# Optimization experiments

Measured on AMD Instinct MI355X. Metric: run time of the kernel, lower is better.

The kernel has to match this reference:

```python
import jax, jax.numpy as jnp
import numpy as np
import math

B, S, DIM = 2, 2048, 2048
H, KV, HD = 16, 1, 128  # query heads, kv heads, head dim


def setup_inputs() -> dict:
    key = jax.random.key(0)
    ks = jax.random.split(key, 6)
    std = 0.02
    return {
        "hidden_states": jax.random.normal(ks[0], (B, S, DIM), jnp.float32),
        "attention_mask": jnp.zeros((B, 1, S, S), jnp.float32),
        "wq": jax.random.normal(ks[1], (DIM, H * HD), jnp.float32) * std,
        "bq": jnp.zeros((H * HD,), jnp.float32),
        "wk": jax.random.normal(ks[2], (DIM, KV * HD), jnp.float32) * std,
        "bk": jnp.zeros((KV * HD,), jnp.float32),
        "wv": jax.random.normal(ks[3], (DIM, KV * HD), jnp.float32) * std,
        "bv": jnp.zeros((KV * HD,), jnp.float32),
        "wo": jax.random.normal(ks[4], (H * HD, DIM), jnp.float32) * std,
        "bo": jnp.zeros((DIM,), jnp.float32),
    }


def reference(hidden_states, attention_mask, wq, bq, wk, bk, wv, bv, wo, bo):
    b, s, _ = hidden_states.shape
    q = (hidden_states @ wq + bq).reshape(b, s, H, HD)
    k = (hidden_states @ wk + bk).reshape(b, s, KV, HD)
    v = (hidden_states @ wv + bv).reshape(b, s, KV, HD)
    # [b, h, s, d]
    q = jnp.transpose(q, (0, 2, 1, 3))
    k = jnp.transpose(k, (0, 2, 1, 3))
    v = jnp.transpose(v, (0, 2, 1, 3))
    # broadcast shared KV heads to all query heads (num_kv_heads < num_query_heads)
    repeats = H // KV
    k = jnp.repeat(k, repeats, axis=1)
    v = jnp.repeat(v, repeats, axis=1)
    scores = jnp.einsum('bhqd,bhkd->bhqk', q, k) / math.sqrt(HD)
    scores = scores + attention_mask
    weights = jax.nn.softmax(scores, axis=-1)
    attn = jnp.einsum('bhqk,bhkd->bhqd', weights, v)
    attn = jnp.transpose(attn, (0, 2, 1, 3)).reshape(b, s, H * HD)
    return attn @ wo + bo
```

## Files before the change

### kernel.cpp

```cpp
#include <hip/hip_runtime.h>
#include <hip/hip_bf16.h>
#include <stdint.h>

#define S_LEN 2048
#define DIMSZ 2048
#define NH    16
#define HD    128
#define NQK   2176
#define NQKV  2304

typedef short  bf16x8  __attribute__((ext_vector_type(8)));
typedef float  floatx4 __attribute__((ext_vector_type(4)));
typedef float  floatx16 __attribute__((ext_vector_type(16)));
typedef int    intx4   __attribute__((ext_vector_type(4)));
typedef unsigned short u16;

#define mfma32 __builtin_amdgcn_mfma_f32_32x32x16_bf16

__device__ __forceinline__ u16 f2bf(float x) {
  unsigned int u = __builtin_bit_cast(unsigned int, x);
  u = (u + 0x7FFFu + ((u >> 16) & 1u)) >> 16;
  return (u16)u;
}

__device__ __forceinline__ int cvtpk(float lo, float hi) {
  int r;
  asm("v_cvt_pk_bf16_f32 %0, %1, %2" : "=v"(r) : "v"(lo), "v"(hi));
  return r;
}

__device__ __forceinline__ void half_swap(int& a, int& b, int lane) {
  int as = __shfl_xor(a, 32);
  int bs = __shfl_xor(b, 32);
  int na = (lane < 32) ? a : bs;
  int nb = (lane < 32) ? as : b;
  a = na; b = nb;
}

__device__ __forceinline__ void gload16(const void* g, void* l) {
  __builtin_amdgcn_global_load_lds(
      reinterpret_cast<const __attribute__((address_space(1))) void*>(reinterpret_cast<uintptr_t>(g)),
      reinterpret_cast<__attribute__((address_space(3))) void*>(reinterpret_cast<uintptr_t>(l)),
      16, 0, 0);
}

__global__ void k_cvt_bf16(const float* __restrict__ in, u16* __restrict__ out, int n4) {
  int i = blockIdx.x * blockDim.x + threadIdx.x;
  if (i < n4) {
    float4 v = ((const float4*)in)[i];
    ushort4 o;
    o.x = f2bf(v.x); o.y = f2bf(v.y); o.z = f2bf(v.z); o.w = f2bf(v.w);
    ((ushort4*)out)[i] = o;
  }
}

__global__ void k_transpose_bf16(const float* __restrict__ in, u16* __restrict__ out,
                                 int K, int N, int rowOff) {
  __shared__ float t[64][65];
  int c0 = blockIdx.x * 64;
  int r0 = blockIdx.y * 64;
  int tid = threadIdx.x;
  int lr = tid >> 6;
  int lc = tid & 63;
#pragma unroll
  for (int i = 0; i < 16; ++i) {
    int r = lr + i * 4;
    t[r][lc] = in[(size_t)(r0 + r) * N + c0 + lc];
  }
  __syncthreads();
#pragma unroll
  for (int i = 0; i < 16; ++i) {
    int r = lr + i * 4;
    out[(size_t)(rowOff + c0 + r) * K + r0 + lc] = f2bf(t[lc][r]);
  }
}

__global__ void k_bias_concat(const float* __restrict__ bq, const float* __restrict__ bk,
                              const float* __restrict__ bv, float* __restrict__ out) {
  int i = blockIdx.x * 256 + threadIdx.x;
  if (i < NQKV) out[i] = (i < 2048) ? bq[i] : (i < NQK ? bk[i - 2048] : bv[i - NQK]);
}

__device__ __forceinline__ void stage_tile(const u16* __restrict__ G, int ldg, int row0, int kt,
                                           u16* lbase, int wid, int lane) {
#pragma unroll
  for (int i = 0; i < 4; ++i) {
    int c   = (wid * 4 + i) * 64 + lane;
    int row = c >> 3, cin = c & 7;
    int cs  = cin ^ (row & 7);
    const u16* g = G + (size_t)(row0 + row) * ldg + kt * 64 + cs * 8;
    gload16(g, (char*)lbase + (wid * 4 + i) * 1024);
  }
}

template <int OMODE>
__global__ __launch_bounds__(256)
void k_gemm(const u16* __restrict__ A, const u16* __restrict__ Bt,
            const float* __restrict__ bias, void* __restrict__ Cout,
            u16* __restrict__ vt, int M, int N, int K) {
  __shared__ u16 lA[2][128 * 64];
  __shared__ u16 lB[2][128 * 64];
  const int tid = threadIdx.x, lane = tid & 63, wid = tid >> 6;
  const int wm = wid >> 1, wn = wid & 1;
  const int tm = blockIdx.x, tn = blockIdx.y;
  const int nk = K >> 6;

  stage_tile(A, K, tm * 128, 0, lA[0], wid, lane);
  stage_tile(Bt, K, tn * 128, 0, lB[0], wid, lane);
  __syncthreads();

  floatx4 acc[4][4] = {};
  int buf = 0;
  for (int kt = 0; kt < nk; ++kt) {
    if (kt + 1 < nk) {
      stage_tile(A, K, tm * 128, kt + 1, lA[buf ^ 1], wid, lane);
      stage_tile(Bt, K, tn * 128, kt + 1, lB[buf ^ 1], wid, lane);
    }
    const char* pa = (const char*)&lA[buf][0];
    const char* pb = (const char*)&lB[buf][0];
#pragma unroll
    for (int kk = 0; kk < 2; ++kk) {
      bf16x8 af[4], bfr[4];
      int gch = kk * 4 + (lane >> 4);
#pragma unroll
      for (int f = 0; f < 4; ++f) {
        int ra = wm * 64 + f * 16 + (lane & 15);
        af[f]  = *(const bf16x8*)(pa + ra * 128 + ((gch ^ (ra & 7)) << 4));
        int rb = wn * 64 + f * 16 + (lane & 15);
        bfr[f] = *(const bf16x8*)(pb + rb * 128 + ((gch ^ (rb & 7)) << 4));
      }
#pragma unroll
      for (int fm = 0; fm < 4; ++fm)
#pragma unroll
        for (int fn = 0; fn < 4; ++fn)
          acc[fm][fn] = __builtin_amdgcn_mfma_f32_16x16x32_bf16(af[fm], bfr[fn], acc[fm][fn], 0, 0, 0);
    }
    __syncthreads();
    buf ^= 1;
  }

#pragma unroll
  for (int fm = 0; fm < 4; ++fm)
#pragma unroll
    for (int fn = 0; fn < 4; ++fn)
#pragma unroll
      for (int r = 0; r < 4; ++r) {
        int rowg = tm * 128 + wm * 64 + fm * 16 + (lane >> 4) * 4 + r;
        int colg = tn * 128 + wn * 64 + fn * 16 + (lane & 15);
        float v = acc[fm][fn][r] + bias[colg];
        if constexpr (OMODE == 1) {
          ((float*)Cout)[(size_t)rowg * N + colg] = v;
        } else {
          if (colg < NQK) {
            ((u16*)Cout)[(size_t)rowg * N + colg] = f2bf(v);
          } else {
            int d = colg - NQK;
            int bg = rowg >> 11, s = rowg & 2047;
            vt[((size_t)bg * HD + d) * S_LEN + s] = f2bf(v);
          }
        }
      }
}

__device__ __forceinline__ void stage_kv(const u16* __restrict__ qkv, const u16* __restrict__ vt,
                                         int b, int kt, u16* lK, u16* lV, int wid, int lane) {
#pragma unroll
  for (int i = 0; i < 2; ++i) {
    int seg = wid * 2 + i;
    {
      int r = seg * 4 + (lane >> 4), cin = lane & 15;
      const u16* g = qkv + (size_t)(b * S_LEN + kt * 64 + r) * NQKV + 2048 + ((cin ^ (r & 7)) * 8);
      gload16(g, (char*)lK + seg * 1024);
    }
    {
      int r = seg * 8 + (lane >> 3), cin = lane & 7;
      const u16* g = vt + ((size_t)b * HD + r) * S_LEN + kt * 64 + ((cin ^ (r & 7)) * 8);
      gload16(g, (char*)lV + seg * 1024);
    }
  }
}

__global__ __launch_bounds__(512)
void k_attn(const u16* __restrict__ qkv, const u16* __restrict__ vt,
            const float* __restrict__ mask, u16* __restrict__ attn) {
  __shared__ __align__(16) u16   lK[2][64 * 128];
  __shared__ __align__(16) u16   lV[2][128 * 64];
  __shared__ __align__(16) float lM[2][32 * 64];
  const int tid = threadIdx.x, lane = tid & 63, wid = tid >> 6;
  const int qt = blockIdx.x, hg = blockIdx.y, b = blockIdx.z;
  const int h = hg * 8 + wid;
  const int q = lane & 31, h5 = lane >> 5;
  const float scale = 0.08838834764831845f;

  bf16x8 qf[8];
  const size_t qrow = (size_t)(b * S_LEN + qt * 32 + q);
#pragma unroll
  for (int cs = 0; cs < 8; ++cs)
    qf[cs] = *(const bf16x8*)(qkv + qrow * NQKV + h * HD + cs * 16 + h5 * 8);

  float m_ = -1e30f, l_ = 0.f;
  floatx16 acco[4] = {};

  const int mq = tid >> 4, mc = tid & 15;
  const float* mrow = mask + (size_t)b * S_LEN * S_LEN + (size_t)(qt * 32 + mq) * S_LEN + mc * 4;

  stage_kv(qkv, vt, b, 0, lK[0], lV[0], wid, lane);
  floatx4 mreg = *(const floatx4*)(mrow);
  *(floatx4*)((char*)&lM[0][0] + mq * 256 + ((mc ^ (mq & 7)) << 4)) = mreg;
  __syncthreads();

  int buf = 0;
  for (int kt = 0; kt < S_LEN / 64; ++kt) {
    if (kt + 1 < S_LEN / 64) {
      stage_kv(qkv, vt, b, kt + 1, lK[buf ^ 1], lV[buf ^ 1], wid, lane);
      mreg = *(const floatx4*)(mrow + (size_t)(kt + 1) * 64);
    }

    floatx16 accs0 = {}, accs1 = {};
    const char* pK = (const char*)&lK[buf][0];
#pragma unroll
    for (int cs = 0; cs < 8; ++cs) {
      int c = cs * 2 + h5;
      bf16x8 kf0 = *(const bf16x8*)(pK + q * 256 + ((c ^ (q & 7)) << 4));
      bf16x8 kf1 = *(const bf16x8*)(pK + (32 + q) * 256 + 8192 - 8192 + ((c ^ (q & 7)) << 4));
      accs0 = mfma32(kf0, qf[cs], accs0, 0, 0, 0);
      accs1 = mfma32(kf1, qf[cs], accs1, 0, 0, 0);
    }

    float pr[32];
    float rowm = -1e30f;
    const char* pM = (const char*)&lM[buf][0];
#pragma unroll
    for (int kb = 0; kb < 2; ++kb)
#pragma unroll
      for (int rg = 0; rg < 4; ++rg) {
        int c = kb * 8 + rg * 2 + h5;
        floatx4 m4 = *(const floatx4*)(pM + q * 256 + ((c ^ (q & 7)) << 4));
#pragma unroll
        for (int t = 0; t < 4; ++t) {
          float sv = (kb ? accs1[rg * 4 + t] : accs0[rg * 4 + t]) * scale + m4[t];
          pr[kb * 16 + rg * 4 + t] = sv;
          rowm = fmaxf(rowm, sv);
        }
      }
    rowm = fmaxf(rowm, __shfl_xor(rowm, 32));
    float mn = fmaxf(m_, rowm);
    float al = __expf(m_ - mn);
    m_ = mn;
    float sum = 0.f;
#pragma unroll
    for (int j = 0; j < 32; ++j) {
      float e = __expf(pr[j] - mn);
      pr[j] = e;
      sum += e;
    }
    sum += __shfl_xor(sum, 32);
    l_ = l_ * al + sum;
#pragma unroll
    for (int dt = 0; dt < 4; ++dt) acco[dt] *= al;

    bf16x8 pf[4];
#pragma unroll
    for (int kb = 0; kb < 2; ++kb)
#pragma unroll
      for (int s = 0; s < 2; ++s) {
        int base = kb * 16 + s * 8;
        int A0 = cvtpk(pr[base + 0], pr[base + 1]);
        int A1 = cvtpk(pr[base + 2], pr[base + 3]);
        int B0 = cvtpk(pr[base + 4], pr[base + 5]);
        int B1 = cvtpk(pr[base + 6], pr[base + 7]);
        half_swap(A0, B0, lane);
        half_swap(A1, B1, lane);
        intx4 w;
        w[0] = A0; w[1] = A1; w[2] = B0; w[3] = B1;
        pf[kb * 2 + s] = __builtin_bit_cast(bf16x8, w);
      }

    const char* pV = (const char*)&lV[buf][0];
#pragma unroll
    for (int dt = 0; dt < 4; ++dt) {
      int rd = dt * 32 + q;
#pragma unroll
      for (int ks = 0; ks < 4; ++ks) {
        int c = ks * 2 + h5;
        bf16x8 vf = *(const bf16x8*)(pV + rd * 128 + ((c ^ (q & 7)) << 4));
        acco[dt] = mfma32(vf, pf[ks], acco[dt], 0, 0, 0);
      }
    }

    if (kt + 1 < S_LEN / 64)
      *(floatx4*)((char*)&lM[buf ^ 1][0] + mq * 256 + ((mc ^ (mq & 7)) << 4)) = mreg;
    __syncthreads();
    buf ^= 1;
  }

  float inv = 1.0f / l_;
  u16* obase = attn + qrow * DIMSZ + h * HD;
#pragma unroll
  for (int dt = 0; dt < 4; ++dt)
#pragma unroll
    for (int rg = 0; rg < 4; ++rg) {
      int d0 = dt * 32 + rg * 8 + h5 * 4;
      ushort4 st;
      st.x = f2bf(acco[dt][rg * 4 + 0] * inv);
      st.y = f2bf(acco[dt][rg * 4 + 1] * inv);
      st.z = f2bf(acco[dt][rg * 4 + 2] * inv);
      st.w = f2bf(acco[dt][rg * 4 + 3] * inv);
      *(ushort4*)(obase + d0) = st;
    }
}

extern "C" void kernel_launch(void* const* d_in, const int* in_sizes, int n_in,
                              void* d_out, int out_size, void* d_ws, size_t ws_size,
                              hipStream_t stream) {
  const float* hidden = (const float*)d_in[0];
  const float* mask   = (const float*)d_in[1];
  const float* wq = (const float*)d_in[2];
  const float* bq = (const float*)d_in[3];
  const float* wk = (const float*)d_in[4];
  const float* bk = (const float*)d_in[5];
  const float* wv = (const float*)d_in[6];
  const float* bv = (const float*)d_in[7];
  const float* wo = (const float*)d_in[8];
  const float* bo = (const float*)d_in[9];
  float* out = (float*)d_out;

  char* ws = (char*)d_ws;
  u16*   hb    = (u16*)(ws);
  u16*   wqkvT = (u16*)(ws + 16777216);
  u16*   woT   = (u16*)(ws + 26214400);
  float* bqkv  = (float*)(ws + 34603008);
  u16*   qkv   = (u16*)(ws + 34612224);
  u16*   vt    = (u16*)(ws + 53486592);
  u16*   attn  = (u16*)(ws + 54535168);

  k_cvt_bf16<<<dim3(8192), dim3(256), 0, stream>>>(hidden, hb, 4096 * 2048 / 4);
  k_transpose_bf16<<<dim3(32, 32), dim3(256), 0, stream>>>(wq, wqkvT, 2048, 2048, 0);
  k_transpose_bf16<<<dim3(2, 32),  dim3(256), 0, stream>>>(wk, wqkvT, 2048, 128, 2048);
  k_transpose_bf16<<<dim3(2, 32),  dim3(256), 0, stream>>>(wv, wqkvT, 2048, 128, NQK);
  k_transpose_bf16<<<dim3(32, 32), dim3(256), 0, stream>>>(wo, woT, 2048, 2048, 0);
  k_bias_concat<<<dim3(9), dim3(256), 0, stream>>>(bq, bk, bv, bqkv);

  k_gemm<0><<<dim3(32, 18), dim3(256), 0, stream>>>(hb, wqkvT, bqkv, (void*)qkv, vt, 4096, NQKV, 2048);
  k_attn<<<dim3(64, 2, 2), dim3(512), 0, stream>>>(qkv, vt, mask, attn);
  k_gemm<1><<<dim3(32, 16), dim3(256), 0, stream>>>(attn, woT, bo, (void*)out, (u16*)nullptr, 4096, 2048, 2048);
}
```

Before: 213.3 us.

## Use exp2 softmax with lazy rescale, permlane32 swaps, and MFMA priority hints

The attention softmax now works in the log2 domain: the scale and the mask are premultiplied by log2(e), and exp2 replaces __expf. The running-max rescale of the output accumulators is skipped unless some row's max grows past a threshold. Cross-half shuffles and reductions use permlane32_swap where the builtin exists, and s_setprio raises wave priority around the MFMA blocks in both the GEMM and attention kernels. The lazy rescale lets exp values exceed 1, up to about 2^11.5, which may affect bf16 precision of P.

```diff
diff --git a/kernel.cpp b/kernel.cpp
--- a/kernel.cpp
+++ b/kernel.cpp
@@ -16,6 +16,7 @@
 typedef unsigned short u16;
 
 #define mfma32 __builtin_amdgcn_mfma_f32_32x32x16_bf16
+#define LOG2E 1.4426950408889634f
 
 __device__ __forceinline__ u16 f2bf(float x) {
   unsigned int u = __builtin_bit_cast(unsigned int, x);
@@ -29,13 +30,39 @@
   return r;
 }
 
-__device__ __forceinline__ void half_swap(int& a, int& b, int lane) {
+#if __has_builtin(__builtin_amdgcn_exp2f)
+__device__ __forceinline__ float fexp2(float x) { return __builtin_amdgcn_exp2f(x); }
+#else
+__device__ __forceinline__ float fexp2(float x) { return exp2f(x); }
+#endif
+
+#if __has_builtin(__builtin_amdgcn_permlane32_swap)
+__device__ __forceinline__ void half_swap(int& a, int& b) {
+  auto r = __builtin_amdgcn_permlane32_swap(a, b, false, false);
+  a = (int)r[0]; b = (int)r[1];
+}
+__device__ __forceinline__ float red_max32(float x) {
+  int xi = __builtin_bit_cast(int, x);
+  auto r = __builtin_amdgcn_permlane32_swap(xi, xi, false, false);
+  return fmaxf(__builtin_bit_cast(float, (int)r[0]), __builtin_bit_cast(float, (int)r[1]));
+}
+__device__ __forceinline__ float red_add32(float x) {
+  int xi = __builtin_bit_cast(int, x);
+  auto r = __builtin_amdgcn_permlane32_swap(xi, xi, false, false);
+  return __builtin_bit_cast(float, (int)r[0]) + __builtin_bit_cast(float, (int)r[1]);
+}
+#else
+__device__ __forceinline__ void half_swap(int& a, int& b) {
   int as = __shfl_xor(a, 32);
   int bs = __shfl_xor(b, 32);
+  int lane = threadIdx.x & 63;
   int na = (lane < 32) ? a : bs;
   int nb = (lane < 32) ? as : b;
   a = na; b = nb;
 }
+__device__ __forceinline__ float red_max32(float x) { return fmaxf(x, __shfl_xor(x, 32)); }
+__device__ __forceinline__ float red_add32(float x) { return x + __shfl_xor(x, 32); }
+#endif
 
 __device__ __forceinline__ void gload16(const void* g, void* l) {
   __builtin_amdgcn_global_load_lds(
@@ -129,11 +156,13 @@
         int rb = wn * 64 + f * 16 + (lane & 15);
         bfr[f] = *(const bf16x8*)(pb + rb * 128 + ((gch ^ (rb & 7)) << 4));
       }
+      __builtin_amdgcn_s_setprio(1);
 #pragma unroll
       for (int fm = 0; fm < 4; ++fm)
 #pragma unroll
         for (int fn = 0; fn < 4; ++fn)
           acc[fm][fn] = __builtin_amdgcn_mfma_f32_16x16x32_bf16(af[fm], bfr[fn], acc[fm][fn], 0, 0, 0);
+      __builtin_amdgcn_s_setprio(0);
     }
     __syncthreads();
     buf ^= 1;
@@ -190,7 +219,7 @@
   const int qt = blockIdx.x, hg = blockIdx.y, b = blockIdx.z;
   const int h = hg * 8 + wid;
   const int q = lane & 31, h5 = lane >> 5;
-  const float scale = 0.08838834764831845f;
+  const float c_sl2 = 0.08838834764831845f * LOG2E;
 
   bf16x8 qf[8];
   const size_t qrow = (size_t)(b * S_LEN + qt * 32 + q);
@@ -206,7 +235,7 @@
 
   stage_kv(qkv, vt, b, 0, lK[0], lV[0], wid, lane);
   floatx4 mreg = *(const floatx4*)(mrow);
-  *(floatx4*)((char*)&lM[0][0] + mq * 256 + ((mc ^ (mq & 7)) << 4)) = mreg;
+  *(floatx4*)((char*)&lM[0][0] + mq * 256 + ((mc ^ (mq & 7)) << 4)) = mreg * LOG2E;
   __syncthreads();
 
   int buf = 0;
@@ -218,14 +247,16 @@
 
     floatx16 accs0 = {}, accs1 = {};
     const char* pK = (const char*)&lK[buf][0];
+    __builtin_amdgcn_s_setprio(1);
 #pragma unroll
     for (int cs = 0; cs < 8; ++cs) {
       int c = cs * 2 + h5;
       bf16x8 kf0 = *(const bf16x8*)(pK + q * 256 + ((c ^ (q & 7)) << 4));
-      bf16x8 kf1 = *(const bf16x8*)(pK + (32 + q) * 256 + 8192 - 8192 + ((c ^ (q & 7)) << 4));
+      bf16x8 kf1 = *(const bf16x8*)(pK + (32 + q) * 256 + ((c ^ (q & 7)) << 4));
       accs0 = mfma32(kf0, qf[cs], accs0, 0, 0, 0);
       accs1 = mfma32(kf1, qf[cs], accs1, 0, 0, 0);
     }
+    __builtin_amdgcn_s_setprio(0);
 
     float pr[32];
     float rowm = -1e30f;
@@ -238,26 +269,28 @@
         floatx4 m4 = *(const floatx4*)(pM + q * 256 + ((c ^ (q & 7)) << 4));
 #pragma unroll
         for (int t = 0; t < 4; ++t) {
-          float sv = (kb ? accs1[rg * 4 + t] : accs0[rg * 4 + t]) * scale + m4[t];
+          float sv = (kb ? accs1[rg * 4 + t] : accs0[rg * 4 + t]) * c_sl2 + m4[t];
           pr[kb * 16 + rg * 4 + t] = sv;
           rowm = fmaxf(rowm, sv);
         }
       }
-    rowm = fmaxf(rowm, __shfl_xor(rowm, 32));
-    float mn = fmaxf(m_, rowm);
-    float al = __expf(m_ - mn);
-    m_ = mn;
+    rowm = red_max32(rowm);
+    if (__any(rowm > m_ + 11.5415603f)) {
+      float mn = fmaxf(m_, rowm);
+      float al = fexp2(m_ - mn);
+      m_ = mn;
+      l_ *= al;
+#pragma unroll
+      for (int dt = 0; dt < 4; ++dt) acco[dt] *= al;
+    }
     float sum = 0.f;
 #pragma unroll
     for (int j = 0; j < 32; ++j) {
-      float e = __expf(pr[j] - mn);
+      float e = fexp2(pr[j] - m_);
       pr[j] = e;
       sum += e;
     }
-    sum += __shfl_xor(sum, 32);
-    l_ = l_ * al + sum;
-#pragma unroll
-    for (int dt = 0; dt < 4; ++dt) acco[dt] *= al;
+    l_ += red_add32(sum);
 
     bf16x8 pf[4];
 #pragma unroll
@@ -269,14 +302,15 @@
         int A1 = cvtpk(pr[base + 2], pr[base + 3]);
         int B0 = cvtpk(pr[base + 4], pr[base + 5]);
         int B1 = cvtpk(pr[base + 6], pr[base + 7]);
-        half_swap(A0, B0, lane);
-        half_swap(A1, B1, lane);
+        half_swap(A0, B0);
+        half_swap(A1, B1);
         intx4 w;
         w[0] = A0; w[1] = A1; w[2] = B0; w[3] = B1;
         pf[kb * 2 + s] = __builtin_bit_cast(bf16x8, w);
       }
 
     const char* pV = (const char*)&lV[buf][0];
+    __builtin_amdgcn_s_setprio(1);
 #pragma unroll
     for (int dt = 0; dt < 4; ++dt) {
       int rd = dt * 32 + q;
@@ -287,9 +321,10 @@
         acco[dt] = mfma32(vf, pf[ks], acco[dt], 0, 0, 0);
       }
     }
+    __builtin_amdgcn_s_setprio(0);
 
     if (kt + 1 < S_LEN / 64)
-      *(floatx4*)((char*)&lM[buf ^ 1][0] + mq * 256 + ((mc ^ (mq & 7)) << 4)) = mreg;
+      *(floatx4*)((char*)&lM[buf ^ 1][0] + mq * 256 + ((mc ^ (mq & 7)) << 4)) = mreg * LOG2E;
     __syncthreads();
     buf ^= 1;
   }
```

Result: faster. 204.7 us (-4.0%).
